# Performance work log

Hardware: AMD Instinct MI355X
Metric: run time of the kernel (lower is better)

Reference implementation:

```python
import jax, jax.numpy as jnp
import numpy as np

N_NODES = 100000
N_EDGES = 3200000
N_FEAT = 128
HIDDEN = 16
N_CLASSES = 10
N_GRAPHS = 512


def setup_inputs() -> dict:
    key = jax.random.key(0)
    ks = jax.random.split(key, 12)
    x = jax.random.normal(ks[0], (N_NODES, N_FEAT), dtype=jnp.float32)
    edge_index = jax.random.randint(ks[1], (2, N_EDGES), 0, N_NODES, dtype=jnp.int64)
    batch = jnp.sort(jax.random.randint(ks[2], (N_NODES,), 0, N_GRAPHS, dtype=jnp.int64))
    def glorot(k, fan_in, fan_out):
        s = jnp.sqrt(6.0 / (fan_in + fan_out)).astype(jnp.float32)
        return jax.random.uniform(k, (fan_in, fan_out), jnp.float32, -s, s)
    W1 = glorot(ks[3], N_FEAT, HIDDEN); b1 = jnp.zeros((HIDDEN,), jnp.float32)
    W2 = glorot(ks[4], HIDDEN, HIDDEN); b2 = jnp.zeros((HIDDEN,), jnp.float32)
    W3 = glorot(ks[5], HIDDEN, HIDDEN); b3 = jnp.zeros((HIDDEN,), jnp.float32)
    Wlin = glorot(ks[6], HIDDEN, N_CLASSES)
    blin = jnp.zeros((N_CLASSES,), jnp.float32)
    return {"x": x, "edge_index": edge_index, "batch": batch,
            "W1": W1, "b1": b1, "W2": W2, "b2": b2, "W3": W3, "b3": b3,
            "Wlin": Wlin, "blin": blin}


def _gcn_conv(x, W, b, src, dst, norm, n):
    # h = X W ; out[dst] += norm * h[src] ; + bias
    h = x @ W
    out = jax.ops.segment_sum(h[src] * norm[:, None], dst, num_segments=n)
    return out + b


def reference(x, edge_index, batch, W1, b1, W2, b2, W3, b3, Wlin, blin):
    n = x.shape[0]
    loop = jnp.arange(n, dtype=edge_index.dtype)
    src = jnp.concatenate([edge_index[0], loop])  # add self-loops (PyG GCNConv default)
    dst = jnp.concatenate([edge_index[1], loop])
    # symmetric degree normalization: deg over destination (incl. self-loops)
    deg = jax.ops.segment_sum(jnp.ones_like(dst, dtype=x.dtype), dst, num_segments=n)
    dinv = jnp.where(deg > 0, jax.lax.rsqrt(jnp.maximum(deg, 1.0)), 0.0)
    norm = dinv[src] * dinv[dst]  # [E+N]

    h = jax.nn.relu(_gcn_conv(x, W1, b1, src, dst, norm, n))
    h = jax.nn.relu(_gcn_conv(h, W2, b2, src, dst, norm, n))
    h = _gcn_conv(h, W3, b3, src, dst, norm, n)
    # global add pool over graphs
    pooled = jax.ops.segment_sum(h, batch, num_segments=N_GRAPHS)  # [G, hidden]
    # dropout p=0.5 is identity in eval mode
    return pooled @ Wlin + blin
```

## Files before the change

### kernel.cpp

```cpp
#include <hip/hip_runtime.h>
#include <hip/hip_fp16.h>

#define N_NODES   100000
#define N_EDGES   3200000
#define N_FEAT    128
#define HIDDEN    16
#define N_CLASSES 10
#define N_GRAPHS  512
#define NPB       256
#define NBUCKET   391
#define EPB       4096
#define PBLK      ((N_EDGES + EPB - 1) / EPB)
#define PSLACK    15872
#define CSLACK    9216


__global__ void cursor_init_kernel(int* __restrict__ cur) {
    int i = blockIdx.x * 256 + threadIdx.x;
    if (i < NBUCKET) cur[i] = i * PSLACK;
}

__global__ __launch_bounds__(512) void partition_kernel(const int* __restrict__ src,
                                                        const int* __restrict__ dst,
                                                        int* __restrict__ cur,
                                                        unsigned* __restrict__ part) {
    __shared__ int cnt[NBUCKET];
    __shared__ int lbase[NBUCKET];
    __shared__ int rk[NBUCKET];
    __shared__ int gbase[NBUCKET];
    __shared__ int s[512];
    __shared__ unsigned sorted[EPB];
    __shared__ unsigned short bb[EPB];
    __shared__ unsigned char  dl[EPB];
    int tid = threadIdx.x;
    for (int i = tid; i < NBUCKET; i += 512) cnt[i] = 0;
    __syncthreads();
    int s0 = blockIdx.x * EPB;
#pragma unroll
    for (int i = 0; i < EPB / 512; ++i) {
        int le = i * 512 + tid;
        int e  = s0 + le;
        if (e < N_EDGES) {
            int d = dst[e];
            int b = d >> 8;
            bb[le] = (unsigned short)b;
            dl[le] = (unsigned char)(d & 255);
            atomicAdd(&cnt[b], 1);
        }
    }
    __syncthreads();
    int v = (tid < NBUCKET) ? cnt[tid] : 0;
    s[tid] = v;
    __syncthreads();
    for (int off = 1; off < 512; off <<= 1) {
        int t = (tid >= off) ? s[tid - off] : 0;
        __syncthreads();
        s[tid] += t;
        __syncthreads();
    }
    if (tid < NBUCKET) {
        int lb = s[tid] - v;
        lbase[tid] = lb;
        rk[tid]    = lb;
        int cpad = (v + 15) & ~15;
        gbase[tid] = cpad ? atomicAdd(&cur[tid], cpad) : 0;
    }
    __syncthreads();
#pragma unroll
    for (int i = 0; i < EPB / 512; ++i) {
        int le = i * 512 + tid;
        int e  = s0 + le;
        if (e < N_EDGES) {
            int b = bb[le];
            int r = atomicAdd(&rk[b], 1);
            sorted[r] = (unsigned)src[e] | ((unsigned)dl[le] << 17);
        }
    }
    __syncthreads();
    int w16 = tid >> 4, l16 = tid & 15;
    for (int b = w16; b < NBUCKET; b += 32) {
        int c = cnt[b];
        if (!c) continue;
        int cpad = (c + 15) & ~15;
        int lb = lbase[b], gb = gbase[b];
        for (int j = l16; j < cpad; j += 16)
            part[gb + j] = (j < c) ? sorted[lb + j] : 0xFFFFFFFFu;
    }
}

__global__ __launch_bounds__(512) void build_csr_kernel(const unsigned* __restrict__ part,
                                                        const int* __restrict__ cur,
                                                        int* __restrict__ rp_beg, int* __restrict__ rp_end,
                                                        float* __restrict__ dinv, int* __restrict__ csr) {
    __shared__ int ncnt[256];
    __shared__ int s[512];
    int b   = blockIdx.x;
    int tid = threadIdx.x;
    int beg = b * PSLACK, end = cur[b];
    if (tid < 256) ncnt[tid] = 0;
    __syncthreads();
    for (int j = beg + tid; j < end; j += 512) {
        unsigned r = part[j];
        if (r != 0xFFFFFFFFu) atomicAdd(&ncnt[(r >> 17) & 255], 1);
    }
    __syncthreads();
    int deg = (tid < 256) ? ncnt[tid] : 0;
    s[tid] = deg;
    __syncthreads();
    for (int off = 1; off < 512; off <<= 1) {
        int t = (tid >= off) ? s[tid - off] : 0;
        __syncthreads();
        s[tid] += t;
        __syncthreads();
    }
    int excl = s[tid] - deg;
    int cbeg = b * CSLACK;
    if (tid < 256) {
        int node = b * 256 + tid;
        if (node < N_NODES) {
            rp_beg[node] = cbeg + excl;
            rp_end[node] = cbeg + excl + deg;
            dinv[node]   = rsqrtf((float)(deg + 1));
        }
    }
    __syncthreads();
    if (tid < 256) ncnt[tid] = cbeg + excl;
    __syncthreads();
    for (int j = beg + tid; j < end; j += 512) {
        unsigned r = part[j];
        if (r != 0xFFFFFFFFu) {
            int vv = (r >> 17) & 255;
            int slot = atomicAdd(&ncnt[vv], 1);
            csr[slot] = (int)(r & 0x1FFFFu);
        }
    }
}


__device__ __forceinline__ void pack_store8(__half* outp, int idx, const float* o) {
    int4 w;
    __half2 q;
    q = __floats2half2_rn(o[0], o[1]); w.x = *(int*)&q;
    q = __floats2half2_rn(o[2], o[3]); w.y = *(int*)&q;
    q = __floats2half2_rn(o[4], o[5]); w.z = *(int*)&q;
    q = __floats2half2_rn(o[6], o[7]); w.w = *(int*)&q;
    ((int4*)outp)[idx] = w;
}

__global__ void transform_x_kernel(const float* __restrict__ x, const float* __restrict__ W,
                                   const float* __restrict__ dinv, __half* __restrict__ g) {
    __shared__ float Wl[N_FEAT * HIDDEN];
    int tid = threadIdx.x;
    for (int i = tid; i < N_FEAT * HIDDEN; i += 256) Wl[i] = W[i];
    __syncthreads();
    int v = blockIdx.x * 256 + tid;
    if (v >= N_NODES) return;
    float acc[HIDDEN];
#pragma unroll
    for (int f = 0; f < HIDDEN; ++f) acc[f] = 0.f;
    const float4* xr = (const float4*)(x + (size_t)v * N_FEAT);
#pragma unroll 4
    for (int k4 = 0; k4 < N_FEAT / 4; ++k4) {
        float4 xv = xr[k4];
        const float* wr = &Wl[k4 * 4 * HIDDEN];
#pragma unroll
        for (int f = 0; f < HIDDEN; ++f)
            acc[f] += xv.x * wr[f] + xv.y * wr[HIDDEN + f] +
                      xv.z * wr[2 * HIDDEN + f] + xv.w * wr[3 * HIDDEN + f];
    }
    float di = dinv[v];
#pragma unroll
    for (int f = 0; f < HIDDEN; ++f) acc[f] *= di;
    pack_store8(g, v * 2,     &acc[0]);
    pack_store8(g, v * 2 + 1, &acc[8]);
}

__global__ void transform_h_kernel(const __half* __restrict__ h, const float* __restrict__ W,
                                   const float* __restrict__ dinv, __half* __restrict__ g) {
    __shared__ float Wl[HIDDEN * HIDDEN];
    int tid = threadIdx.x;
    if (tid < HIDDEN * HIDDEN) Wl[tid] = W[tid];
    __syncthreads();
    int v = blockIdx.x * 256 + tid;
    if (v >= N_NODES) return;
    int4 r0 = ((const int4*)h)[v * 2];
    int4 r1 = ((const int4*)h)[v * 2 + 1];
    float hv[HIDDEN];
    {
        const int rr[8] = {r0.x, r0.y, r0.z, r0.w, r1.x, r1.y, r1.z, r1.w};
#pragma unroll
        for (int q = 0; q < 8; ++q) {
            __half2 p = *(const __half2*)&rr[q];
            float2 f2 = __half22float2(p);
            hv[q * 2] = f2.x; hv[q * 2 + 1] = f2.y;
        }
    }
    float acc[HIDDEN];
#pragma unroll
    for (int f = 0; f < HIDDEN; ++f) acc[f] = 0.f;
#pragma unroll
    for (int k = 0; k < HIDDEN; ++k) {
        float hk = hv[k];
#pragma unroll
        for (int f = 0; f < HIDDEN; ++f) acc[f] += hk * Wl[k * HIDDEN + f];
    }
    float di = dinv[v];
#pragma unroll
    for (int f = 0; f < HIDDEN; ++f) acc[f] *= di;
    pack_store8(g, v * 2,     &acc[0]);
    pack_store8(g, v * 2 + 1, &acc[8]);
}

__global__ void aggregate_kernel(const __half* __restrict__ g, const int* __restrict__ rp_beg,
                                 const int* __restrict__ rp_end, const int* __restrict__ csr,
                                 const float* __restrict__ dinv, const float* __restrict__ bias,
                                 __half* __restrict__ hout, int do_relu) {
    int tid  = threadIdx.x;
    int wave = tid >> 6;
    int l    = tid & 63;
    int c  = l >> 3;
    int vl = (l >> 1) & 3;
    int hh = l & 1;
    int v = blockIdx.x * 16 + wave * 4 + vl;
    if (v >= N_NODES) return;
    int beg = rp_beg[v];
    int deg = rp_end[v] - beg;
    int j0 = beg + ((deg * c) >> 3);
    int j1 = beg + ((deg * (c + 1)) >> 3);
    const int4* g4 = (const int4*)g;
    float a0 = 0.f, a1 = 0.f, a2 = 0.f, a3 = 0.f, a4 = 0.f, a5 = 0.f, a6 = 0.f, a7 = 0.f;
#pragma unroll 4
    for (int j = j0; j < j1; ++j) {
        int s = csr[j];
        int4 r = g4[s * 2 + hh];
        float2 f0 = __half22float2(*(const __half2*)&r.x);
        float2 f1 = __half22float2(*(const __half2*)&r.y);
        float2 f2 = __half22float2(*(const __half2*)&r.z);
        float2 f3 = __half22float2(*(const __half2*)&r.w);
        a0 += f0.x; a1 += f0.y; a2 += f1.x; a3 += f1.y;
        a4 += f2.x; a5 += f2.y; a6 += f3.x; a7 += f3.y;
    }
    a0 += __shfl_xor(a0, 8);  a1 += __shfl_xor(a1, 8);
    a2 += __shfl_xor(a2, 8);  a3 += __shfl_xor(a3, 8);
    a4 += __shfl_xor(a4, 8);  a5 += __shfl_xor(a5, 8);
    a6 += __shfl_xor(a6, 8);  a7 += __shfl_xor(a7, 8);
    a0 += __shfl_xor(a0, 16); a1 += __shfl_xor(a1, 16);
    a2 += __shfl_xor(a2, 16); a3 += __shfl_xor(a3, 16);
    a4 += __shfl_xor(a4, 16); a5 += __shfl_xor(a5, 16);
    a6 += __shfl_xor(a6, 16); a7 += __shfl_xor(a7, 16);
    a0 += __shfl_xor(a0, 32); a1 += __shfl_xor(a1, 32);
    a2 += __shfl_xor(a2, 32); a3 += __shfl_xor(a3, 32);
    a4 += __shfl_xor(a4, 32); a5 += __shfl_xor(a5, 32);
    a6 += __shfl_xor(a6, 32); a7 += __shfl_xor(a7, 32);
    if (c == 0) {
        int4 r = g4[v * 2 + hh];
        float2 s0 = __half22float2(*(const __half2*)&r.x);
        float2 s1 = __half22float2(*(const __half2*)&r.y);
        float2 s2 = __half22float2(*(const __half2*)&r.z);
        float2 s3 = __half22float2(*(const __half2*)&r.w);
        float di = dinv[v];
        const float4* bp = (const float4*)bias;
        float4 bA = bp[hh * 2];
        float4 bB = bp[hh * 2 + 1];
        float o[8];
        o[0] = di * (a0 + s0.x) + bA.x;
        o[1] = di * (a1 + s0.y) + bA.y;
        o[2] = di * (a2 + s1.x) + bA.z;
        o[3] = di * (a3 + s1.y) + bA.w;
        o[4] = di * (a4 + s2.x) + bB.x;
        o[5] = di * (a5 + s2.y) + bB.y;
        o[6] = di * (a6 + s3.x) + bB.z;
        o[7] = di * (a7 + s3.y) + bB.w;
        if (do_relu) {
#pragma unroll
            for (int i = 0; i < 8; ++i) o[i] = fmaxf(o[i], 0.f);
        }
        pack_store8(hout, v * 2 + hh, o);
    }
}


__global__ void pool_head_kernel(const __half* __restrict__ h, const int* __restrict__ batch,
                                 const float* __restrict__ Wlin, const float* __restrict__ blin,
                                 float* __restrict__ out) {
    __shared__ float red[256];
    __shared__ int bounds[2];
    int g   = blockIdx.x;
    int tid = threadIdx.x;
    if (tid < 2) {
        int target = g + tid;
        int lo = 0, hi = N_NODES;
        while (lo < hi) {
            int mid = (lo + hi) >> 1;
            if (batch[mid] < target) lo = mid + 1; else hi = mid;
        }
        bounds[tid] = lo;
    }
    __syncthreads();
    int start = bounds[0], end = bounds[1];
    int f = tid & 15, r = tid >> 4;
    float acc = 0.f;
    for (int v = start + r; v < end; v += 16)
        acc += __half2float(h[v * HIDDEN + f]);
    red[tid] = acc;
    __syncthreads();
    for (int off = 128; off >= 16; off >>= 1) {
        if (tid < off) red[tid] += red[tid + off];
        __syncthreads();
    }
    if (tid < N_CLASSES) {
        float s = blin[tid];
#pragma unroll
        for (int fe = 0; fe < HIDDEN; ++fe) s += red[fe] * Wlin[fe * N_CLASSES + tid];
        out[g * N_CLASSES + tid] = s;
    }
}


extern "C" void kernel_launch(void* const* d_in, const int* in_sizes, int n_in,
                              void* d_out, int out_size, void* d_ws, size_t ws_size,
                              hipStream_t stream) {
    const float* x     = (const float*)d_in[0];
    const int*   ei    = (const int*)d_in[1];
    const int*   src   = ei;
    const int*   dst   = ei + N_EDGES;
    const int*   batch = (const int*)d_in[2];
    const float* W1 = (const float*)d_in[3];
    const float* b1 = (const float*)d_in[4];
    const float* W2 = (const float*)d_in[5];
    const float* b2 = (const float*)d_in[6];
    const float* W3 = (const float*)d_in[7];
    const float* b3 = (const float*)d_in[8];
    const float* Wlin = (const float*)d_in[9];
    const float* blin = (const float*)d_in[10];
    float* out = (float*)d_out;

    char* w = (char*)d_ws;
    auto alloc = [&](size_t bytes) -> char* {
        char* p = w;
        w += (bytes + 255) & ~(size_t)255;
        return p;
    };
    int*    cur    = (int*)alloc((size_t)NBUCKET * 4);
    int*    rp_beg = (int*)alloc((size_t)N_NODES * 4);
    int*    rp_end = (int*)alloc((size_t)N_NODES * 4);
    float*  dinv   = (float*)alloc((size_t)N_NODES * 4);
    __half* g      = (__half*)alloc((size_t)N_NODES * HIDDEN * 2);
    __half* hA     = (__half*)alloc((size_t)N_NODES * HIDDEN * 2);
    __half* hB     = (__half*)alloc((size_t)N_NODES * HIDDEN * 2);
    unsigned* part = (unsigned*)alloc((size_t)NBUCKET * PSLACK * 4);
    int*    csr    = (int*)alloc((size_t)NBUCKET * CSLACK * 4);

    int nbn = (N_NODES + 255) / 256;
    int ab  = (N_NODES + 15) / 16;

    cursor_init_kernel<<<(NBUCKET + 255) / 256, 256, 0, stream>>>(cur);
    partition_kernel<<<PBLK, 512, 0, stream>>>(src, dst, cur, part);
    build_csr_kernel<<<NBUCKET, 512, 0, stream>>>(part, cur, rp_beg, rp_end, dinv, csr);

    transform_x_kernel<<<nbn, 256, 0, stream>>>(x, W1, dinv, g);
    aggregate_kernel<<<ab, 256, 0, stream>>>(g, rp_beg, rp_end, csr, dinv, b1, hA, 1);
    transform_h_kernel<<<nbn, 256, 0, stream>>>(hA, W2, dinv, g);
    aggregate_kernel<<<ab, 256, 0, stream>>>(g, rp_beg, rp_end, csr, dinv, b2, hB, 1);
    transform_h_kernel<<<nbn, 256, 0, stream>>>(hB, W3, dinv, g);
    aggregate_kernel<<<ab, 256, 0, stream>>>(g, rp_beg, rp_end, csr, dinv, b3, hA, 0);

    pool_head_kernel<<<N_GRAPHS, 256, 0, stream>>>(hA, batch, Wlin, blin, out);
}
```

Measured before the change: 275.0 us.

## Fuse next-layer hidden transform into aggregation epilogue, pack row pointers

Folds the 16x16 hidden-layer weight transform (plus dinv scaling) into the epilogue of the aggregation kernel, with the two half-row lanes combining partial products via a lane shuffle. This removes two transform kernel launches and their full read/write passes over the node features. Row pointers are packed into int2 so each node needs one load, and edges are now split across the eight lanes in a strided pattern instead of contiguous chunks. The early return for out-of-range nodes was removed, but N_NODES divides evenly by 16, so it is safe here.

```diff
diff --git a/kernel.cpp b/kernel.cpp
--- a/kernel.cpp
+++ b/kernel.cpp
@@ -90,7 +90,7 @@
 
 __global__ __launch_bounds__(512) void build_csr_kernel(const unsigned* __restrict__ part,
                                                         const int* __restrict__ cur,
-                                                        int* __restrict__ rp_beg, int* __restrict__ rp_end,
+                                                        int2* __restrict__ rp,
                                                         float* __restrict__ dinv, int* __restrict__ csr) {
     __shared__ int ncnt[256];
     __shared__ int s[512];
@@ -118,9 +118,8 @@
     if (tid < 256) {
         int node = b * 256 + tid;
         if (node < N_NODES) {
-            rp_beg[node] = cbeg + excl;
-            rp_end[node] = cbeg + excl + deg;
-            dinv[node]   = rsqrtf((float)(deg + 1));
+            rp[node]   = make_int2(cbeg + excl, cbeg + excl + deg);
+            dinv[node] = rsqrtf((float)(deg + 1));
         }
     }
     __syncthreads();
@@ -175,62 +174,30 @@
     pack_store8(g, v * 2 + 1, &acc[8]);
 }
 
-__global__ void transform_h_kernel(const __half* __restrict__ h, const float* __restrict__ W,
-                                   const float* __restrict__ dinv, __half* __restrict__ g) {
-    __shared__ float Wl[HIDDEN * HIDDEN];
-    int tid = threadIdx.x;
-    if (tid < HIDDEN * HIDDEN) Wl[tid] = W[tid];
-    __syncthreads();
-    int v = blockIdx.x * 256 + tid;
-    if (v >= N_NODES) return;
-    int4 r0 = ((const int4*)h)[v * 2];
-    int4 r1 = ((const int4*)h)[v * 2 + 1];
-    float hv[HIDDEN];
-    {
-        const int rr[8] = {r0.x, r0.y, r0.z, r0.w, r1.x, r1.y, r1.z, r1.w};
-#pragma unroll
-        for (int q = 0; q < 8; ++q) {
-            __half2 p = *(const __half2*)&rr[q];
-            float2 f2 = __half22float2(p);
-            hv[q * 2] = f2.x; hv[q * 2 + 1] = f2.y;
-        }
-    }
-    float acc[HIDDEN];
-#pragma unroll
-    for (int f = 0; f < HIDDEN; ++f) acc[f] = 0.f;
-#pragma unroll
-    for (int k = 0; k < HIDDEN; ++k) {
-        float hk = hv[k];
-#pragma unroll
-        for (int f = 0; f < HIDDEN; ++f) acc[f] += hk * Wl[k * HIDDEN + f];
-    }
-    float di = dinv[v];
-#pragma unroll
-    for (int f = 0; f < HIDDEN; ++f) acc[f] *= di;
-    pack_store8(g, v * 2,     &acc[0]);
-    pack_store8(g, v * 2 + 1, &acc[8]);
-}
-
-__global__ void aggregate_kernel(const __half* __restrict__ g, const int* __restrict__ rp_beg,
-                                 const int* __restrict__ rp_end, const int* __restrict__ csr,
-                                 const float* __restrict__ dinv, const float* __restrict__ bias,
-                                 __half* __restrict__ hout, int do_relu) {
+template <int MODE>
+__global__ __launch_bounds__(256) void aggregate_kernel(
+        const __half* __restrict__ g, const int2* __restrict__ rp,
+        const int* __restrict__ csr, const float* __restrict__ dinv,
+        const float* __restrict__ bias, const float* __restrict__ Wn,
+        __half* __restrict__ out) {
+    __shared__ float WnL[HIDDEN * HIDDEN];
     int tid  = threadIdx.x;
+    if (MODE == 2) {
+        if (tid < HIDDEN * HIDDEN) WnL[tid] = Wn[tid];
+        __syncthreads();
+    }
     int wave = tid >> 6;
     int l    = tid & 63;
     int c  = l >> 3;
     int vl = (l >> 1) & 3;
     int hh = l & 1;
     int v = blockIdx.x * 16 + wave * 4 + vl;
-    if (v >= N_NODES) return;
-    int beg = rp_beg[v];
-    int deg = rp_end[v] - beg;
-    int j0 = beg + ((deg * c) >> 3);
-    int j1 = beg + ((deg * (c + 1)) >> 3);
+    int2 range = rp[v];
+    int beg = range.x, end = range.y;
     const int4* g4 = (const int4*)g;
     float a0 = 0.f, a1 = 0.f, a2 = 0.f, a3 = 0.f, a4 = 0.f, a5 = 0.f, a6 = 0.f, a7 = 0.f;
 #pragma unroll 4
-    for (int j = j0; j < j1; ++j) {
+    for (int j = beg + c; j < end; j += 8) {
         int s = csr[j];
         int4 r = g4[s * 2 + hh];
         float2 f0 = __half22float2(*(const __half2*)&r.x);
@@ -271,11 +238,33 @@
         o[5] = di * (a5 + s2.y) + bB.y;
         o[6] = di * (a6 + s3.x) + bB.z;
         o[7] = di * (a7 + s3.y) + bB.w;
-        if (do_relu) {
+        if (MODE == 2) {
 #pragma unroll
             for (int i = 0; i < 8; ++i) o[i] = fmaxf(o[i], 0.f);
-        }
-        pack_store8(hout, v * 2 + hh, o);
+            float pa[16];
+#pragma unroll
+            for (int f = 0; f < 16; ++f) pa[f] = 0.f;
+            const float* wr = &WnL[hh * 8 * HIDDEN];
+#pragma unroll
+            for (int q = 0; q < 8; ++q) {
+                float hq = o[q];
+#pragma unroll
+                for (int f = 0; f < 16; ++f) pa[f] += hq * wr[q * HIDDEN + f];
+            }
+            float o2[8];
+#pragma unroll
+            for (int i = 0; i < 8; ++i) {
+                float lo = pa[i];
+                float hi = pa[8 + i];
+                float keep = hh ? hi : lo;
+                float send = hh ? lo : hi;
+                float recv = __shfl_xor(send, 1);
+                o2[i] = di * (keep + recv);
+            }
+            pack_store8(out, v * 2 + hh, o2);
+        } else {
+            pack_store8(out, v * 2 + hh, o);
+        }
     }
 }
 
@@ -342,12 +331,11 @@
         return p;
     };
     int*    cur    = (int*)alloc((size_t)NBUCKET * 4);
-    int*    rp_beg = (int*)alloc((size_t)N_NODES * 4);
-    int*    rp_end = (int*)alloc((size_t)N_NODES * 4);
+    int2*   rp     = (int2*)alloc((size_t)N_NODES * 8);
     float*  dinv   = (float*)alloc((size_t)N_NODES * 4);
-    __half* g      = (__half*)alloc((size_t)N_NODES * HIDDEN * 2);
+    __half* gA     = (__half*)alloc((size_t)N_NODES * HIDDEN * 2);
+    __half* gB     = (__half*)alloc((size_t)N_NODES * HIDDEN * 2);
     __half* hA     = (__half*)alloc((size_t)N_NODES * HIDDEN * 2);
-    __half* hB     = (__half*)alloc((size_t)N_NODES * HIDDEN * 2);
     unsigned* part = (unsigned*)alloc((size_t)NBUCKET * PSLACK * 4);
     int*    csr    = (int*)alloc((size_t)NBUCKET * CSLACK * 4);
 
@@ -356,14 +344,12 @@
 
     cursor_init_kernel<<<(NBUCKET + 255) / 256, 256, 0, stream>>>(cur);
     partition_kernel<<<PBLK, 512, 0, stream>>>(src, dst, cur, part);
-    build_csr_kernel<<<NBUCKET, 512, 0, stream>>>(part, cur, rp_beg, rp_end, dinv, csr);
-
-    transform_x_kernel<<<nbn, 256, 0, stream>>>(x, W1, dinv, g);
-    aggregate_kernel<<<ab, 256, 0, stream>>>(g, rp_beg, rp_end, csr, dinv, b1, hA, 1);
-    transform_h_kernel<<<nbn, 256, 0, stream>>>(hA, W2, dinv, g);
-    aggregate_kernel<<<ab, 256, 0, stream>>>(g, rp_beg, rp_end, csr, dinv, b2, hB, 1);
-    transform_h_kernel<<<nbn, 256, 0, stream>>>(hB, W3, dinv, g);
-    aggregate_kernel<<<ab, 256, 0, stream>>>(g, rp_beg, rp_end, csr, dinv, b3, hA, 0);
+    build_csr_kernel<<<NBUCKET, 512, 0, stream>>>(part, cur, rp, dinv, csr);
+
+    transform_x_kernel<<<nbn, 256, 0, stream>>>(x, W1, dinv, gA);
+    aggregate_kernel<2><<<ab, 256, 0, stream>>>(gA, rp, csr, dinv, b1, W2, gB);
+    aggregate_kernel<2><<<ab, 256, 0, stream>>>(gB, rp, csr, dinv, b2, W3, gA);
+    aggregate_kernel<0><<<ab, 256, 0, stream>>>(gA, rp, csr, dinv, b3, nullptr, hA);
 
     pool_head_kernel<<<N_GRAPHS, 256, 0, stream>>>(hA, batch, Wlin, blin, out);
 }
```

Measured after the change: 270.5 us. Within noise of the previous version (-1.6%).
